# Optimization experiments

Measured on AMD Instinct MI355X. Metric: run time of the kernel, lower is better.

## Reference

```python
import jax, jax.numpy as jnp
import numpy as np

D_MODEL = 1024
H = 16
D_HEAD = D_MODEL // H
EPS = 1e-5  # torch LayerNorm default


def setup_inputs() -> dict:
    key = jax.random.key(0)
    ks = jax.random.split(key, 10)
    bs, seq = 4, 2048
    scale = 1.0 / np.sqrt(D_MODEL)
    return {
        "q": jax.random.normal(ks[0], (bs, seq, D_MODEL), jnp.float32),
        "k": jax.random.normal(ks[1], (bs, seq, D_MODEL), jnp.float32),
        "v": jax.random.normal(ks[2], (bs, seq, D_MODEL), jnp.float32),
        "zero_mask": jnp.zeros((bs, 1, 1, seq), jnp.float32),
        "Wq": jax.random.normal(ks[3], (D_MODEL, D_MODEL), jnp.float32) * scale,
        "Wk": jax.random.normal(ks[4], (D_MODEL, D_MODEL), jnp.float32) * scale,
        "Wv": jax.random.normal(ks[5], (D_MODEL, D_MODEL), jnp.float32) * scale,
        "Wo": jax.random.normal(ks[6], (D_MODEL, D_MODEL), jnp.float32) * scale,
        "gamma": jnp.ones((D_MODEL,), jnp.float32),
        "beta": jnp.zeros((D_MODEL,), jnp.float32),
    }


def reference(q, k, v, zero_mask, Wq, Wk, Wv, Wo, gamma, beta):
    bs, seq_q, _ = q.shape
    seq_k = k.shape[1]
    residual = q
    # Projections (torch Linear: x @ W.T), split into heads -> (bs, h, seq, d)
    qh = (q @ Wq.T).reshape(bs, seq_q, H, D_HEAD).transpose(0, 2, 1, 3)
    kh = (k @ Wk.T).reshape(bs, seq_k, H, D_HEAD).transpose(0, 2, 1, 3)
    vh = (v @ Wv.T).reshape(bs, seq_k, H, D_HEAD).transpose(0, 2, 1, 3)
    # Scaled dot-product attention with additive -1e9 * zero_mask
    att = jnp.einsum("bhqd,bhkd->bhqk", qh, kh) / np.sqrt(D_HEAD)
    att = att + zero_mask * -1e9
    att = jax.nn.softmax(att, axis=-1)
    # dropout: identity in eval-mode reference
    ctx = jnp.einsum("bhqk,bhkd->bhqd", att, vh)
    ctx = ctx.transpose(0, 2, 1, 3).reshape(bs, seq_q, D_MODEL)
    out = ctx @ Wo.T
    out = out + residual
    # LayerNorm over last dim
    mu = jnp.mean(out, axis=-1, keepdims=True)
    var = jnp.var(out, axis=-1, keepdims=True)
    out = (out - mu) * jax.lax.rsqrt(var + EPS) * gamma + beta
    return out
```

## Files before the change

kernel.cpp:

```cpp
#include <hip/hip_runtime.h>
#include <hip/hip_bf16.h>

typedef __bf16 bf16x8 __attribute__((ext_vector_type(8)));
typedef float  f32x4  __attribute__((ext_vector_type(4)));
typedef short  s16x4  __attribute__((ext_vector_type(4)));

#define D_MODEL 1024
#define SEQ 2048
#define BS 4
#define NH 16
#define DH 64
#define MTOT (BS * SEQ)

#define AS1 __attribute__((address_space(1)))
#define AS3 __attribute__((address_space(3)))

template <typename T>
__device__ inline bf16x8 ld8(const T* p);

template <>
__device__ inline bf16x8 ld8<float>(const float* p) {
    f32x4 a = *(const f32x4*)p;
    f32x4 b = *(const f32x4*)(p + 4);
    bf16x8 r;
    r[0] = (__bf16)a[0]; r[1] = (__bf16)a[1]; r[2] = (__bf16)a[2]; r[3] = (__bf16)a[3];
    r[4] = (__bf16)b[0]; r[5] = (__bf16)b[1]; r[6] = (__bf16)b[2]; r[7] = (__bf16)b[3];
    return r;
}

template <>
__device__ inline bf16x8 ld8<__bf16>(const __bf16* p) {
    return *(const bf16x8*)p;
}

__global__ __launch_bounds__(256) void cvt4_kernel(
    const float* __restrict__ a, const float* __restrict__ b,
    const float* __restrict__ c, const float* __restrict__ e,
    __bf16* __restrict__ x, __bf16* __restrict__ y,
    __bf16* __restrict__ z, __bf16* __restrict__ w)
{
    const float* s = (blockIdx.y == 0) ? a : (blockIdx.y == 1) ? b : (blockIdx.y == 2) ? c : e;
    __bf16*      d = (blockIdx.y == 0) ? x : (blockIdx.y == 1) ? y : (blockIdx.y == 2) ? z : w;
    const long i = ((long)blockIdx.x * 256 + threadIdx.x) * 8;
    *(bf16x8*)(d + i) = ld8<float>(s + i);
}

__global__ __launch_bounds__(256) void gemm_qkv(
    const float* __restrict__ q, const float* __restrict__ k, const float* __restrict__ v,
    const __bf16* __restrict__ Wb,
    __bf16* __restrict__ Qp, __bf16* __restrict__ Kp, __bf16* __restrict__ Vp)
{
    __shared__ __align__(16) __bf16 As[2 * 4096];
    __shared__ __align__(16) __bf16 Bs[2 * 4096];
    const int K = D_MODEL, N = D_MODEL;
    const int z = blockIdx.z;
    const float* A = (z == 0) ? q : (z == 1) ? k : v;
    const __bf16* B = Wb + (long)z * D_MODEL * D_MODEL;
    __bf16* C = (z == 0) ? Qp : (z == 1) ? Kp : Vp;

    const int t = threadIdx.x;
    const int wave = t >> 6, lane = t & 63;
    const int quad = lane >> 4, l15 = lane & 15;
    const int wm = (wave >> 1) * 64, wn = (wave & 1) * 64;
    const long m0 = (long)blockIdx.x * 128;
    const long n0 = (long)blockIdx.y * 128;
    const int sr = t >> 2, sc = (t & 3) * 8;

    const __bf16* gB = B + (n0 + sr) * (long)K + sc;
    __bf16* lB0 = Bs + wave * 512;
    __bf16* lB1 = Bs + 2048 + wave * 512;
    __bf16* lB2 = Bs + 4096 + wave * 512;
    __bf16* lB3 = Bs + 6144 + wave * 512;

    f32x4 acc[4][4] = {};

    for (int k0 = 0; k0 < K; k0 += 64) {
        __builtin_amdgcn_global_load_lds((const AS1 void*)(gB + k0),               (AS3 void*)lB0, 16, 0, 0);
        __builtin_amdgcn_global_load_lds((const AS1 void*)(gB + 64 * K + k0),      (AS3 void*)lB1, 16, 0, 0);
        __builtin_amdgcn_global_load_lds((const AS1 void*)(gB + k0 + 32),          (AS3 void*)lB2, 16, 0, 0);
        __builtin_amdgcn_global_load_lds((const AS1 void*)(gB + 64 * K + k0 + 32), (AS3 void*)lB3, 16, 0, 0);
        *(bf16x8*)&As[sr * 32 + sc]               = ld8<float>(&A[(m0 + sr) * K + k0 + sc]);
        *(bf16x8*)&As[(sr + 64) * 32 + sc]        = ld8<float>(&A[(m0 + sr + 64) * K + k0 + sc]);
        *(bf16x8*)&As[4096 + sr * 32 + sc]        = ld8<float>(&A[(m0 + sr) * K + k0 + 32 + sc]);
        *(bf16x8*)&As[4096 + (sr + 64) * 32 + sc] = ld8<float>(&A[(m0 + sr + 64) * K + k0 + 32 + sc]);
        __syncthreads();
#pragma unroll
        for (int p = 0; p < 2; ++p) {
            bf16x8 af[4], bfr[4];
#pragma unroll
            for (int i = 0; i < 4; ++i) af[i]  = *(const bf16x8*)&As[p * 4096 + (wm + i * 16 + l15) * 32 + quad * 8];
#pragma unroll
            for (int i = 0; i < 4; ++i) bfr[i] = *(const bf16x8*)&Bs[p * 4096 + (wn + i * 16 + l15) * 32 + quad * 8];
#pragma unroll
            for (int i = 0; i < 4; ++i)
#pragma unroll
                for (int j = 0; j < 4; ++j)
                    acc[i][j] = __builtin_amdgcn_mfma_f32_16x16x32_bf16(af[i], bfr[j], acc[i][j], 0, 0, 0);
        }
        __syncthreads();
    }

#pragma unroll
    for (int i = 0; i < 4; ++i)
#pragma unroll
        for (int j = 0; j < 4; ++j) {
            const long r = m0 + wm + i * 16 + quad * 4;
            const long c = n0 + wn + j * 16 + l15;
#pragma unroll
            for (int reg = 0; reg < 4; ++reg)
                C[(r + reg) * N + c] = (__bf16)acc[i][j][reg];
        }
}

__global__ __launch_bounds__(256) void gemm_bb(
    const __bf16* __restrict__ A, const __bf16* __restrict__ B,
    __bf16* __restrict__ C, int M, int N, int K)
{
    __shared__ __align__(16) __bf16 As[2 * 4096];
    __shared__ __align__(16) __bf16 Bs[2 * 4096];
    const int t = threadIdx.x;
    const int wave = t >> 6, lane = t & 63;
    const int quad = lane >> 4, l15 = lane & 15;
    const int wm = (wave >> 1) * 64, wn = (wave & 1) * 64;
    const long m0 = (long)blockIdx.x * 128;
    const long n0 = (long)blockIdx.y * 128;
    const int sr = t >> 2, sc = (t & 3) * 8;

    const __bf16* gA = A + (m0 + sr) * (long)K + sc;
    const __bf16* gB = B + (n0 + sr) * (long)K + sc;
    __bf16* lA0 = As + wave * 512;
    __bf16* lA1 = As + 2048 + wave * 512;
    __bf16* lA2 = As + 4096 + wave * 512;
    __bf16* lA3 = As + 6144 + wave * 512;
    __bf16* lB0 = Bs + wave * 512;
    __bf16* lB1 = Bs + 2048 + wave * 512;
    __bf16* lB2 = Bs + 4096 + wave * 512;
    __bf16* lB3 = Bs + 6144 + wave * 512;

    f32x4 acc[4][4] = {};

    for (int k0 = 0; k0 < K; k0 += 64) {
        __builtin_amdgcn_global_load_lds((const AS1 void*)(gA + k0),               (AS3 void*)lA0, 16, 0, 0);
        __builtin_amdgcn_global_load_lds((const AS1 void*)(gA + 64 * K + k0),      (AS3 void*)lA1, 16, 0, 0);
        __builtin_amdgcn_global_load_lds((const AS1 void*)(gA + k0 + 32),          (AS3 void*)lA2, 16, 0, 0);
        __builtin_amdgcn_global_load_lds((const AS1 void*)(gA + 64 * K + k0 + 32), (AS3 void*)lA3, 16, 0, 0);
        __builtin_amdgcn_global_load_lds((const AS1 void*)(gB + k0),               (AS3 void*)lB0, 16, 0, 0);
        __builtin_amdgcn_global_load_lds((const AS1 void*)(gB + 64 * K + k0),      (AS3 void*)lB1, 16, 0, 0);
        __builtin_amdgcn_global_load_lds((const AS1 void*)(gB + k0 + 32),          (AS3 void*)lB2, 16, 0, 0);
        __builtin_amdgcn_global_load_lds((const AS1 void*)(gB + 64 * K + k0 + 32), (AS3 void*)lB3, 16, 0, 0);
        __syncthreads();
#pragma unroll
        for (int p = 0; p < 2; ++p) {
            bf16x8 af[4], bfr[4];
#pragma unroll
            for (int i = 0; i < 4; ++i) af[i]  = *(const bf16x8*)&As[p * 4096 + (wm + i * 16 + l15) * 32 + quad * 8];
#pragma unroll
            for (int i = 0; i < 4; ++i) bfr[i] = *(const bf16x8*)&Bs[p * 4096 + (wn + i * 16 + l15) * 32 + quad * 8];
#pragma unroll
            for (int i = 0; i < 4; ++i)
#pragma unroll
                for (int j = 0; j < 4; ++j)
                    acc[i][j] = __builtin_amdgcn_mfma_f32_16x16x32_bf16(af[i], bfr[j], acc[i][j], 0, 0, 0);
        }
        __syncthreads();
    }

#pragma unroll
    for (int i = 0; i < 4; ++i)
#pragma unroll
        for (int j = 0; j < 4; ++j) {
            const long r = m0 + wm + i * 16 + quad * 4;
            const long c = n0 + wn + j * 16 + l15;
#pragma unroll
            for (int reg = 0; reg < 4; ++reg)
                C[(r + reg) * N + c] = (__bf16)acc[i][j][reg];
        }
}

__global__ __launch_bounds__(256) void attn_kernel(
    const __bf16* Qp, const __bf16* __restrict__ Kp, const __bf16* __restrict__ Vp,
    const float* __restrict__ mask, __bf16* Ctx)
{
    __shared__ __align__(16) __bf16 Ks[2][64][72];
    __shared__ __align__(16) __bf16 Vt[2][64][76];
    __shared__ __align__(16) float  Ms[2][64];

    const int t = threadIdx.x;
    const int wave = t >> 6, lane = t & 63;
    const int quad = lane >> 4, l15 = lane & 15;
    const int qt = blockIdx.x;
    const int bh = blockIdx.y;
    const int b = bh >> 4, h = bh & 15;
    const long rowbase = (long)b * SEQ;
    const int q0 = qt * 128 + wave * 16;

    bf16x8 aq[2][2];
#pragma unroll
    for (int qi = 0; qi < 2; ++qi) {
        const long qrow = rowbase + q0 + qi * 64 + l15;
        const __bf16* qptr = Qp + qrow * D_MODEL + h * DH + quad * 8;
        aq[qi][0] = *(const bf16x8*)(qptr);
        aq[qi][1] = *(const bf16x8*)(qptr + 32);
    }

    const s16x4 ones = {(short)0x3F80, (short)0x3F80, (short)0x3F80, (short)0x3F80};

    f32x4 acc_l[2] = {};
    f32x4 acc_o[2][4] = {};

    const int sr = t >> 2, sc = (t & 3) * 16;
    const int kp2 = (t >> 3) * 2, dc = (t & 7) * 8;
    const float C1 = 0.125f * 1.44269504f;
    const float C2 = -1e9f * 1.44269504f;

    const __bf16* kbase = Kp + (rowbase + sr) * D_MODEL + h * DH + sc;
    const __bf16* vbase = Vp + (rowbase + kp2) * D_MODEL + h * DH + dc;

    bf16x8 kr0 = *(const bf16x8*)(kbase);
    bf16x8 kr1 = *(const bf16x8*)(kbase + 8);
    bf16x8 vr0 = *(const bf16x8*)(vbase);
    bf16x8 vr1 = *(const bf16x8*)(vbase + D_MODEL);
    float  mreg = (t < 64) ? mask[rowbase + t] * C2 : 0.f;

    for (int kt = 0; kt < SEQ / 64; ++kt) {
        const int buf = kt & 1;
        *(bf16x8*)&Ks[buf][sr][sc]     = kr0;
        *(bf16x8*)&Ks[buf][sr][sc + 8] = kr1;
#pragma unroll
        for (int e = 0; e < 8; ++e) {
            union { __bf16 h2[2]; unsigned u; } pk;
            pk.h2[0] = vr0[e]; pk.h2[1] = vr1[e];
            *(unsigned*)&Vt[buf][dc + e][kp2] = pk.u;
        }
        if (t < 64) Ms[buf][t] = mreg;
        __syncthreads();

        {
            const int ktn = (kt + 1 < SEQ / 64) ? kt + 1 : kt;
            const long off = (long)ktn * 64 * D_MODEL;
            kr0 = *(const bf16x8*)(kbase + off);
            kr1 = *(const bf16x8*)(kbase + off + 8);
            vr0 = *(const bf16x8*)(vbase + off);
            vr1 = *(const bf16x8*)(vbase + off + D_MODEL);
            mreg = (t < 64) ? mask[rowbase + ktn * 64 + t] * C2 : 0.f;
        }

        bf16x8 kf[4][2];
#pragma unroll
        for (int nt = 0; nt < 4; ++nt)
#pragma unroll
            for (int ks = 0; ks < 2; ++ks)
                kf[nt][ks] = *(const bf16x8*)&Ks[buf][nt * 16 + l15][ks * 32 + quad * 8];
        s16x4 vtf[4][4];
#pragma unroll
        for (int nt = 0; nt < 4; ++nt)
#pragma unroll
            for (int dt = 0; dt < 4; ++dt)
                vtf[nt][dt] = *(const s16x4*)&Vt[buf][dt * 16 + l15][nt * 16 + quad * 4];
        f32x4 mv[4];
#pragma unroll
        for (int nt = 0; nt < 4; ++nt)
            mv[nt] = *(const f32x4*)&Ms[buf][nt * 16 + quad * 4];

#pragma unroll
        for (int qi = 0; qi < 2; ++qi) {
            f32x4 st[4] = {};
#pragma unroll
            for (int ks = 0; ks < 2; ++ks)
#pragma unroll
                for (int nt = 0; nt < 4; ++nt)
                    st[nt] = __builtin_amdgcn_mfma_f32_16x16x32_bf16(kf[nt][ks], aq[qi][ks], st[nt], 0, 0, 0);
            s16x4 pp[4];
#pragma unroll
            for (int nt = 0; nt < 4; ++nt) {
                float pv0 = __builtin_amdgcn_exp2f(fmaf(st[nt][0], C1, mv[nt][0]));
                float pv1 = __builtin_amdgcn_exp2f(fmaf(st[nt][1], C1, mv[nt][1]));
                float pv2 = __builtin_amdgcn_exp2f(fmaf(st[nt][2], C1, mv[nt][2]));
                float pv3 = __builtin_amdgcn_exp2f(fmaf(st[nt][3], C1, mv[nt][3]));
                union { __hip_bfloat162 h2[2]; s16x4 s; } u;
                u.h2[0] = __float22bfloat162_rn(float2{pv0, pv1});
                u.h2[1] = __float22bfloat162_rn(float2{pv2, pv3});
                pp[nt] = u.s;
            }
#pragma unroll
            for (int nt = 0; nt < 4; ++nt) {
#pragma unroll
                for (int dt = 0; dt < 4; ++dt)
                    acc_o[qi][dt] = __builtin_amdgcn_mfma_f32_16x16x16bf16_1k(pp[nt], vtf[nt][dt], acc_o[qi][dt], 0, 0, 0);
                acc_l[qi] = __builtin_amdgcn_mfma_f32_16x16x16bf16_1k(pp[nt], ones, acc_l[qi], 0, 0, 0);
            }
        }
    }

#pragma unroll
    for (int qi = 0; qi < 2; ++qi)
#pragma unroll
        for (int reg = 0; reg < 4; ++reg) {
            const float inv = 1.f / acc_l[qi][reg];
            const long row = rowbase + q0 + qi * 64 + quad * 4 + reg;
#pragma unroll
            for (int dt = 0; dt < 4; ++dt)
                Ctx[row * D_MODEL + h * DH + dt * 16 + l15] = (__bf16)(acc_o[qi][dt][reg] * inv);
        }
}

__global__ __launch_bounds__(256) void ln_kernel(
    const __bf16* __restrict__ Y, const float* __restrict__ R,
    const float* __restrict__ gamma, const float* __restrict__ beta,
    float* __restrict__ Out)
{
    __shared__ float red[8];
    const long row = blockIdx.x;
    const int t = threadIdx.x;
    const int wave = t >> 6, lane = t & 63;
    float x[4];
    float s = 0.f, s2 = 0.f;
#pragma unroll
    for (int i = 0; i < 4; ++i) {
        const int idx = i * 256 + t;
        const float v = (float)Y[row * D_MODEL + idx] + R[row * D_MODEL + idx];
        x[i] = v; s += v; s2 += v * v;
    }
#pragma unroll
    for (int off = 32; off >= 1; off >>= 1) {
        s  += __shfl_xor(s, off, 64);
        s2 += __shfl_xor(s2, off, 64);
    }
    if (lane == 0) { red[wave] = s; red[4 + wave] = s2; }
    __syncthreads();
    s  = red[0] + red[1] + red[2] + red[3];
    s2 = red[4] + red[5] + red[6] + red[7];
    const float mu   = s * (1.f / 1024.f);
    const float var  = s2 * (1.f / 1024.f) - mu * mu;
    const float rstd = rsqrtf(var + 1e-5f);
#pragma unroll
    for (int i = 0; i < 4; ++i) {
        const int idx = i * 256 + t;
        Out[row * D_MODEL + idx] = (x[i] - mu) * rstd * gamma[idx] + beta[idx];
    }
}

extern "C" void kernel_launch(void* const* d_in, const int* in_sizes, int n_in,
                              void* d_out, int out_size, void* d_ws, size_t ws_size,
                              hipStream_t stream)
{
    const float* q     = (const float*)d_in[0];
    const float* k     = (const float*)d_in[1];
    const float* v     = (const float*)d_in[2];
    const float* mask  = (const float*)d_in[3];
    const float* Wq    = (const float*)d_in[4];
    const float* Wk    = (const float*)d_in[5];
    const float* Wv    = (const float*)d_in[6];
    const float* Wo    = (const float*)d_in[7];
    const float* gamma = (const float*)d_in[8];
    const float* beta  = (const float*)d_in[9];
    float* out = (float*)d_out;

    const long NACT = (long)MTOT * D_MODEL;
    const long NW   = (long)D_MODEL * D_MODEL;

    __bf16* Qp = (__bf16*)d_ws;
    __bf16* Kp = Qp + NACT;
    __bf16* Vp = (__bf16*)d_out;
    __bf16* Wb = Vp + NACT;
    __bf16 *Wqb = Wb, *Wkb = Wb + NW, *Wvb = Wb + 2 * NW, *Wob = Wb + 3 * NW;
    __bf16* Y = Kp;

    cvt4_kernel<<<dim3(NW / 2048, 4), 256, 0, stream>>>(Wq, Wk, Wv, Wo, Wqb, Wkb, Wvb, Wob);

    gemm_qkv<<<dim3(MTOT / 128, D_MODEL / 128, 3), 256, 0, stream>>>(q, k, v, Wqb, Qp, Kp, Vp);

    attn_kernel<<<dim3(SEQ / 128, BS * NH), 256, 0, stream>>>(Qp, Kp, Vp, mask, Qp);

    gemm_bb<<<dim3(MTOT / 128, D_MODEL / 128), 256, 0, stream>>>(Qp, Wob, Y, MTOT, D_MODEL, D_MODEL);

    ln_kernel<<<MTOT, 256, 0, stream>>>(Y, q, gamma, beta, out);
}
```

Before: 366.2 us.

## Interleave QK MFMA with softmax exp across query sub-tiles in attention

Restructures the attention inner loop so the score MFMAs for the second 16-row query sub-tile run alongside the exp/convert of the first, and the PV MFMAs for the first overlap the exp of the second. The intent is to hide transcendental latency behind matrix-core work. s_setprio raises wave priority during the compute section. The grid is also reordered so heads vary fastest, and launch bounds request 4 blocks per CU, which could add register pressure or spills.

```diff
diff --git a/kernel.cpp b/kernel.cpp
--- a/kernel.cpp
+++ b/kernel.cpp
@@ -177,7 +177,18 @@
         }
 }
 
-__global__ __launch_bounds__(256) void attn_kernel(
+__device__ inline s16x4 exp_quad(const f32x4 st, const f32x4 mv, float C1) {
+    float p0 = __builtin_amdgcn_exp2f(fmaf(st[0], C1, mv[0]));
+    float p1 = __builtin_amdgcn_exp2f(fmaf(st[1], C1, mv[1]));
+    float p2 = __builtin_amdgcn_exp2f(fmaf(st[2], C1, mv[2]));
+    float p3 = __builtin_amdgcn_exp2f(fmaf(st[3], C1, mv[3]));
+    union { __hip_bfloat162 h2[2]; s16x4 s; } u;
+    u.h2[0] = __float22bfloat162_rn(float2{p0, p1});
+    u.h2[1] = __float22bfloat162_rn(float2{p2, p3});
+    return u.s;
+}
+
+__global__ __launch_bounds__(256, 4) void attn_kernel(
     const __bf16* Qp, const __bf16* __restrict__ Kp, const __bf16* __restrict__ Vp,
     const float* __restrict__ mask, __bf16* Ctx)
 {
@@ -188,8 +199,8 @@
     const int t = threadIdx.x;
     const int wave = t >> 6, lane = t & 63;
     const int quad = lane >> 4, l15 = lane & 15;
-    const int qt = blockIdx.x;
-    const int bh = blockIdx.y;
+    const int bh = blockIdx.x;
+    const int qt = blockIdx.y;
     const int b = bh >> 4, h = bh & 15;
     const long rowbase = (long)b * SEQ;
     const int q0 = qt * 128 + wave * 16;
@@ -262,34 +273,36 @@
         for (int nt = 0; nt < 4; ++nt)
             mv[nt] = *(const f32x4*)&Ms[buf][nt * 16 + quad * 4];
 
-#pragma unroll
-        for (int qi = 0; qi < 2; ++qi) {
-            f32x4 st[4] = {};
-#pragma unroll
-            for (int ks = 0; ks < 2; ++ks)
-#pragma unroll
-                for (int nt = 0; nt < 4; ++nt)
-                    st[nt] = __builtin_amdgcn_mfma_f32_16x16x32_bf16(kf[nt][ks], aq[qi][ks], st[nt], 0, 0, 0);
-            s16x4 pp[4];
-#pragma unroll
-            for (int nt = 0; nt < 4; ++nt) {
-                float pv0 = __builtin_amdgcn_exp2f(fmaf(st[nt][0], C1, mv[nt][0]));
-                float pv1 = __builtin_amdgcn_exp2f(fmaf(st[nt][1], C1, mv[nt][1]));
-                float pv2 = __builtin_amdgcn_exp2f(fmaf(st[nt][2], C1, mv[nt][2]));
-                float pv3 = __builtin_amdgcn_exp2f(fmaf(st[nt][3], C1, mv[nt][3]));
-                union { __hip_bfloat162 h2[2]; s16x4 s; } u;
-                u.h2[0] = __float22bfloat162_rn(float2{pv0, pv1});
-                u.h2[1] = __float22bfloat162_rn(float2{pv2, pv3});
-                pp[nt] = u.s;
-            }
-#pragma unroll
-            for (int nt = 0; nt < 4; ++nt) {
-#pragma unroll
-                for (int dt = 0; dt < 4; ++dt)
-                    acc_o[qi][dt] = __builtin_amdgcn_mfma_f32_16x16x16bf16_1k(pp[nt], vtf[nt][dt], acc_o[qi][dt], 0, 0, 0);
-                acc_l[qi] = __builtin_amdgcn_mfma_f32_16x16x16bf16_1k(pp[nt], ones, acc_l[qi], 0, 0, 0);
-            }
-        }
+        f32x4 st0[4] = {}, st1[4] = {};
+        s16x4 pp0[4], pp1[4];
+        __builtin_amdgcn_s_setprio(1);
+#pragma unroll
+        for (int ks = 0; ks < 2; ++ks)
+#pragma unroll
+            for (int nt = 0; nt < 4; ++nt)
+                st0[nt] = __builtin_amdgcn_mfma_f32_16x16x32_bf16(kf[nt][ks], aq[0][ks], st0[nt], 0, 0, 0);
+#pragma unroll
+        for (int nt = 0; nt < 4; ++nt) {
+            st1[nt] = __builtin_amdgcn_mfma_f32_16x16x32_bf16(kf[nt][0], aq[1][0], st1[nt], 0, 0, 0);
+            st1[nt] = __builtin_amdgcn_mfma_f32_16x16x32_bf16(kf[nt][1], aq[1][1], st1[nt], 0, 0, 0);
+            pp0[nt] = exp_quad(st0[nt], mv[nt], C1);
+        }
+#pragma unroll
+        for (int nt = 0; nt < 4; ++nt) {
+#pragma unroll
+            for (int dt = 0; dt < 4; ++dt)
+                acc_o[0][dt] = __builtin_amdgcn_mfma_f32_16x16x16bf16_1k(pp0[nt], vtf[nt][dt], acc_o[0][dt], 0, 0, 0);
+            acc_l[0] = __builtin_amdgcn_mfma_f32_16x16x16bf16_1k(pp0[nt], ones, acc_l[0], 0, 0, 0);
+            pp1[nt] = exp_quad(st1[nt], mv[nt], C1);
+        }
+#pragma unroll
+        for (int nt = 0; nt < 4; ++nt) {
+#pragma unroll
+            for (int dt = 0; dt < 4; ++dt)
+                acc_o[1][dt] = __builtin_amdgcn_mfma_f32_16x16x16bf16_1k(pp1[nt], vtf[nt][dt], acc_o[1][dt], 0, 0, 0);
+            acc_l[1] = __builtin_amdgcn_mfma_f32_16x16x16bf16_1k(pp1[nt], ones, acc_l[1], 0, 0, 0);
+        }
+        __builtin_amdgcn_s_setprio(0);
     }
 
 #pragma unroll
@@ -370,7 +383,7 @@
 
     gemm_qkv<<<dim3(MTOT / 128, D_MODEL / 128, 3), 256, 0, stream>>>(q, k, v, Wqb, Qp, Kp, Vp);
 
-    attn_kernel<<<dim3(SEQ / 128, BS * NH), 256, 0, stream>>>(Qp, Kp, Vp, mask, Qp);
+    attn_kernel<<<dim3(BS * NH, SEQ / 128), 256, 0, stream>>>(Qp, Kp, Vp, mask, Qp);
 
     gemm_bb<<<dim3(MTOT / 128, D_MODEL / 128), 256, 0, stream>>>(Qp, Wob, Y, MTOT, D_MODEL, D_MODEL);
 
```

Measured after the change: 862.2 us. 135% more time.
